# Kernel tuning notes

Measured on AMD Instinct MI355X. Metric: run time of the kernel, lower is better.

## Reference

```python
import jax, jax.numpy as jnp
import numpy as np

B, S, D, H = 4, 2048, 768, 12
DK = D // H


def setup_inputs() -> dict:
    key = jax.random.key(0)
    ks = jax.random.split(key, 5)
    sc = 0.02
    return {
        "x": jax.random.normal(ks[0], (B, S, D), dtype=jnp.float32),
        "wq": jax.random.normal(ks[1], (D, D), dtype=jnp.float32) * sc,
        "bq": jnp.zeros((D,), dtype=jnp.float32),
        "wk": jax.random.normal(ks[2], (D, D), dtype=jnp.float32) * sc,
        "bk": jnp.zeros((D,), dtype=jnp.float32),
        "wv": jax.random.normal(ks[3], (D, D), dtype=jnp.float32) * sc,
        "bv": jnp.zeros((D,), dtype=jnp.float32),
        "wo": jax.random.normal(ks[4], (D, D), dtype=jnp.float32) * sc,
        "bo": jnp.zeros((D,), dtype=jnp.float32),
    }


def reference(x, wq, bq, wk, bk, wv, bv, wo, bo):
    b, s, d = x.shape
    # torch nn.Linear: y = x @ W.T + b
    q = (x @ wq.T + bq).reshape(b, s, H, DK).transpose(0, 2, 1, 3)  # [b,h,s,dk]
    k = (x @ wk.T + bk).reshape(b, s, H, DK).transpose(0, 2, 1, 3)
    v = (x @ wv.T + bv).reshape(b, s, H, DK).transpose(0, 2, 1, 3)
    scale = 1.0 / np.sqrt(DK).astype(np.float32)
    scores = jnp.einsum("bhqd,bhkd->bhqk", q, k) * scale  # [b,h,s,s]
    causal = jnp.triu(jnp.ones((s, s), dtype=bool), k=1)  # True above diagonal -> masked
    scores = jnp.where(causal[None, None], jnp.float32(-jnp.inf), scores)
    probs = jax.nn.softmax(scores, axis=-1)
    attn = jnp.einsum("bhqk,bhkd->bhqd", probs, v)  # [b,h,s,dk]
    attn = attn.transpose(0, 2, 1, 3).reshape(b, s, d)
    return attn @ wo.T + bo
```

## Files before the change

kernel.cpp:

```cpp
#include <hip/hip_runtime.h>
#include <hip/hip_bf16.h>
#include <cstdint>

static constexpr int B_ = 4, S_ = 2048, D_ = 768, H_ = 12, DK_ = 64;
static constexpr int M_ = B_ * S_;

typedef short bf16x4 __attribute__((ext_vector_type(4)));
typedef short bf16x8 __attribute__((ext_vector_type(8)));
typedef float f32x4 __attribute__((ext_vector_type(4)));
typedef float f32x16 __attribute__((ext_vector_type(16)));
typedef int i32x4 __attribute__((ext_vector_type(4)));

#define MFMA16(a, b, c) __builtin_amdgcn_mfma_f32_16x16x32_bf16((a), (b), (c), 0, 0, 0)
#define MFMA32(a, b, c) __builtin_amdgcn_mfma_f32_32x32x16_bf16((a), (b), (c), 0, 0, 0)

__device__ inline ushort f2bf(float f) {
  uint32_t u = __float_as_uint(f);
  u += 0x7fffu + ((u >> 16) & 1u);
  return (ushort)(u >> 16);
}
__device__ inline uint32_t pkbf(float a, float b) {
  return (uint32_t)f2bf(a) | ((uint32_t)f2bf(b) << 16);
}
__device__ inline uint32_t cvtpk(float lo, float hi) {
  uint32_t r;
  asm("v_cvt_pk_bf16_f32 %0, %1, %2" : "=v"(r) : "v"(lo), "v"(hi));
  return r;
}
__device__ inline void gload_lds16(const void* g, void* l) {
  __builtin_amdgcn_global_load_lds((const __attribute__((address_space(1))) void*)g,
                                   (__attribute__((address_space(3))) void*)l, 16, 0, 0);
}

__global__ void cvt_f32_bf16(const float* __restrict__ in, ushort* __restrict__ out, int n8) {
  int i = blockIdx.x * 256 + threadIdx.x;
  if (i >= n8) return;
  const float4* p = (const float4*)in;
  float4 v0 = p[2 * i], v1 = p[2 * i + 1];
  ((uint4*)out)[i] = make_uint4(pkbf(v0.x, v0.y), pkbf(v0.z, v0.w),
                                pkbf(v1.x, v1.y), pkbf(v1.z, v1.w));
}

__global__ void cvtw_f32_bf16(const float* __restrict__ w0, const float* __restrict__ w1,
                              const float* __restrict__ w2, const float* __restrict__ w3,
                              ushort* __restrict__ o0, ushort* __restrict__ o1,
                              ushort* __restrict__ o2, ushort* __restrict__ o3, int n8) {
  const float* in;
  ushort* out;
  switch (blockIdx.y) {
    case 0: in = w0; out = o0; break;
    case 1: in = w1; out = o1; break;
    case 2: in = w2; out = o2; break;
    default: in = w3; out = o3; break;
  }
  int i = blockIdx.x * 256 + threadIdx.x;
  if (i >= n8) return;
  const float4* p = (const float4*)in;
  float4 v0 = p[2 * i], v1 = p[2 * i + 1];
  ((uint4*)out)[i] = make_uint4(pkbf(v0.x, v0.y), pkbf(v0.z, v0.w),
                                pkbf(v1.x, v1.y), pkbf(v1.z, v1.w));
}

__global__ __launch_bounds__(256) void gemm_qkv(const ushort* __restrict__ A,
                                                const ushort* __restrict__ Wq,
                                                const ushort* __restrict__ Wk,
                                                const ushort* __restrict__ Wv,
                                                const float* __restrict__ bqp,
                                                const float* __restrict__ bkp,
                                                const float* __restrict__ bvp,
                                                ushort* __restrict__ Qo,
                                                ushort* __restrict__ Ko,
                                                ushort* __restrict__ Vo) {
  constexpr int K = D_;
  constexpr int BK = 64;
  constexpr int NT = K / BK;
  __shared__ ushort SMEM[24576];
  ushort* Asb = SMEM;
  ushort* Bsb = SMEM + 8192;

  const int wsel = blockIdx.y / 6;
  const int bn = (blockIdx.y % 6) * 128;
  const ushort* Bw = wsel == 0 ? Wq : wsel == 1 ? Wk : Wv;
  const float* bias = wsel == 0 ? bqp : wsel == 1 ? bkp : bvp;
  ushort* outp = wsel == 0 ? Qo : wsel == 1 ? Ko : Vo;

  const int tid = threadIdx.x;
  const int lane = tid & 63, w = tid >> 6;
  const int wr = w >> 1, wc = w & 1;
  const int l15 = lane & 15, l4 = lane >> 4;
  const int bm = blockIdx.x * 64;

  const char* Ac = (const char*)A;
  const char* Bc = (const char*)Bw;

  f32x4 acc[2][4] = {};

  auto stage = [&](int buf, int k0) {
#pragma unroll
    for (int i = 0; i < 2; ++i) {
      int o = (i * 256 + tid) * 16;
      int r = o >> 7, c = o & 127;
      int cs = c ^ ((r & 7) << 4);
      gload_lds16(Ac + ((size_t)(bm + r) * K + k0) * 2 + cs,
                  (char*)(Asb + buf * 4096) + o);
    }
#pragma unroll
    for (int i = 0; i < 4; ++i) {
      int o = (i * 256 + tid) * 16;
      int r = o >> 7, c = o & 127;
      int cs = c ^ ((r & 7) << 4);
      gload_lds16(Bc + ((size_t)(bn + r) * K + k0) * 2 + cs,
                  (char*)(Bsb + buf * 8192) + o);
    }
  };

  stage(0, 0);
  __syncthreads();
  int cur = 0;
  for (int t = 0; t < NT; ++t) {
    if (t + 1 < NT) stage(cur ^ 1, (t + 1) * BK);
    const char* Ab = (const char*)(Asb + cur * 4096);
    const char* Bb = (const char*)(Bsb + cur * 8192);
    bf16x8 a[2][2], b[2][4];
#pragma unroll
    for (int kc = 0; kc < 2; ++kc) {
#pragma unroll
      for (int mi = 0; mi < 2; ++mi) {
        int row = wr * 32 + mi * 16 + l15;
        int col = (kc * 64 + l4 * 16) ^ ((row & 7) << 4);
        a[kc][mi] = *(const bf16x8*)(Ab + row * 128 + col);
      }
#pragma unroll
      for (int ni = 0; ni < 4; ++ni) {
        int row = wc * 64 + ni * 16 + l15;
        int col = (kc * 64 + l4 * 16) ^ ((row & 7) << 4);
        b[kc][ni] = *(const bf16x8*)(Bb + row * 128 + col);
      }
    }
    __builtin_amdgcn_s_setprio(1);
    if (wsel < 2) {
#pragma unroll
      for (int kc = 0; kc < 2; ++kc)
#pragma unroll
        for (int mi = 0; mi < 2; ++mi)
#pragma unroll
          for (int ni = 0; ni < 4; ++ni)
            acc[mi][ni] = MFMA16(a[kc][mi], b[kc][ni], acc[mi][ni]);
    } else {
#pragma unroll
      for (int kc = 0; kc < 2; ++kc)
#pragma unroll
        for (int mi = 0; mi < 2; ++mi)
#pragma unroll
          for (int ni = 0; ni < 4; ++ni)
            acc[mi][ni] = MFMA16(b[kc][ni], a[kc][mi], acc[mi][ni]);
    }
    __builtin_amdgcn_s_setprio(0);
    __syncthreads();
    cur ^= 1;
  }

  ushort* Cst = SMEM;
#pragma unroll
  for (int ni = 0; ni < 4; ++ni) {
    float bv[4];
    if (wsel < 2) {
      float bc = bias[bn + wc * 64 + ni * 16 + l15];
#pragma unroll
      for (int r = 0; r < 4; ++r) bv[r] = bc;
    } else {
#pragma unroll
      for (int r = 0; r < 4; ++r) bv[r] = bias[bn + wc * 64 + ni * 16 + l4 * 4 + r];
    }
#pragma unroll
    for (int mi = 0; mi < 2; ++mi)
#pragma unroll
      for (int r = 0; r < 4; ++r) {
        float v = acc[mi][ni][r] + bv[r];
        if (wsel < 2) {
          int lr = wr * 32 + mi * 16 + l4 * 4 + r;
          int lc = wc * 64 + ni * 16 + l15;
          Cst[lr * 128 + (lc ^ ((lr & 3) << 4))] = f2bf(v);
        } else {
          int lr = wc * 64 + ni * 16 + l4 * 4 + r;
          int lc = wr * 32 + mi * 16 + l15;
          Cst[lr * 64 + (lc ^ ((lr & 3) << 4))] = f2bf(v);
        }
      }
  }
  __syncthreads();
  const int bbV = bm >> 11;
#pragma unroll
  for (int it = 0; it < 4; ++it) {
    int chunk = it * 256 + tid;
    if (wsel < 2) {
      int lr = chunk >> 4, cc = chunk & 15;
      i32x4 v = *(const i32x4*)&Cst[lr * 128 + ((cc * 8) ^ ((lr & 3) << 4))];
      int gr = bm + lr;
      int b0 = gr >> 11, s = gr & 2047;
      int gc = bn + cc * 8;
      int h = gc >> 6, dk0 = gc & 63;
      *(i32x4*)&outp[((((size_t)b0 * H_ + h) * S_ + s) << 6) + dk0] = v;
    } else {
      int lr = chunk >> 3, cc = chunk & 7;
      i32x4 v = *(const i32x4*)&Cst[lr * 64 + ((cc * 8) ^ ((lr & 3) << 4))];
      int gn = bn + lr;
      int h = gn >> 6, dk = gn & 63;
      int s0 = (bm & 2047) + cc * 8;
      *(i32x4*)&outp[(((size_t)bbV * H_ + h) * 64 + dk) * S_ + s0] = v;
    }
  }
}

__global__ __launch_bounds__(256) void gemm_out(const ushort* __restrict__ A,
                                                const ushort* __restrict__ Bw,
                                                const float* __restrict__ bias,
                                                float* __restrict__ outp) {
  constexpr int K = D_;
  constexpr int BK = 32;
  constexpr int NT = K / BK;
  __shared__ ushort As[2][64 * BK];
  __shared__ ushort Bs[2][128 * BK];

  const int tid = threadIdx.x;
  const int lane = tid & 63, w = tid >> 6;
  const int wr = w >> 1, wc = w & 1;
  const int l15 = lane & 15, l4 = lane >> 4;
  const int bm = blockIdx.x * 64, bn = blockIdx.y * 128;

  f32x4 acc[2][4] = {};

  auto stage = [&](int buf, int k0) {
    {
      int e = tid * 8;
      int r = e >> 5, c = e & 31;
      gload_lds16(&A[(size_t)(bm + r) * K + k0 + c], &As[buf][e]);
    }
#pragma unroll
    for (int i = 0; i < 2; ++i) {
      int e = (i * 256 + tid) * 8;
      int r = e >> 5, c = e & 31;
      gload_lds16(&Bw[(size_t)(bn + r) * K + k0 + c], &Bs[buf][e]);
    }
  };

  stage(0, 0);
  __syncthreads();
  int cur = 0;
  for (int t = 0; t < NT; ++t) {
    if (t + 1 < NT) stage(cur ^ 1, (t + 1) * BK);
    bf16x8 a[2], b[4];
#pragma unroll
    for (int mi = 0; mi < 2; ++mi)
      a[mi] = *(const bf16x8*)&As[cur][(wr * 32 + mi * 16 + l15) * BK + l4 * 8];
#pragma unroll
    for (int ni = 0; ni < 4; ++ni)
      b[ni] = *(const bf16x8*)&Bs[cur][(wc * 64 + ni * 16 + l15) * BK + l4 * 8];
    __builtin_amdgcn_s_setprio(1);
#pragma unroll
    for (int mi = 0; mi < 2; ++mi)
#pragma unroll
      for (int ni = 0; ni < 4; ++ni)
        acc[mi][ni] = MFMA16(a[mi], b[ni], acc[mi][ni]);
    __builtin_amdgcn_s_setprio(0);
    __syncthreads();
    cur ^= 1;
  }

#pragma unroll
  for (int mi = 0; mi < 2; ++mi)
#pragma unroll
    for (int ni = 0; ni < 4; ++ni) {
      int col = bn + wc * 64 + ni * 16 + l15;
      float bv = bias[col];
#pragma unroll
      for (int r = 0; r < 4; ++r) {
        int row = bm + wr * 32 + mi * 16 + l4 * 4 + r;
        outp[(size_t)row * D_ + col] = acc[mi][ni][r] + bv;
      }
    }
}

__global__ __launch_bounds__(512) void attn_fwd5(const ushort* __restrict__ Q,
                                                 const ushort* __restrict__ Kg,
                                                 const ushort* __restrict__ Vt,
                                                 ushort* __restrict__ Oa) {
  __shared__ ushort KVb[2][2][64 * 64];
  __shared__ float Ml[4][32], Ll[4][32];

  const int bh = blockIdx.x;
  const int w = threadIdx.x >> 6, lane = threadIdx.x & 63;
  const int l31 = lane & 31, hi = lane >> 5;
  const int pair = w >> 1, sp = w & 1;
  const int qtb = gridDim.y - 1 - blockIdx.y;
  const int qb = qtb * 128;
  const int q0 = qb + pair * 32;

  const ushort* Qb = Q + (size_t)bh * (S_ * DK_);
  const char* Kc = (const char*)(Kg + (size_t)bh * (S_ * DK_));
  const char* Vc = (const char*)(Vt + (size_t)bh * (DK_ * S_));
  char* kKT = (char*)&KVb[0][0][0];
  char* kVT = (char*)&KVb[1][0][0];

  bf16x8 qf[4];
#pragma unroll
  for (int kc = 0; kc < 4; ++kc)
    qf[kc] = *(const bf16x8*)&Qb[(q0 + l31) * 64 + kc * 16 + hi * 8];

  f32x16 ot[2] = {};
  float m = -__builtin_inff(), l = 0.f;
  const float C = 0.125f * 1.4426950408889634f;
  const float THR = 8.0f / C;

  auto stage = [&](int buf, int kt) {
    const int k0 = kt * 64;
    int obase = w * 1024;
    int o = obase + lane * 16;
    int mk = ((o >> 7) & 7) << 4;
    gload_lds16(Kc + (size_t)k0 * 128 + (o ^ mk), kKT + buf * 8192 + obase);
    int d = o >> 7, colb = (o & 127) ^ mk;
    gload_lds16(Vc + (size_t)d * 4096 + (size_t)k0 * 2 + colb, kVT + buf * 8192 + obase);
  };

  const int nkt = qb / 64 + 2;
  int cur = 0;
  stage(0, 0);
  __syncthreads();

  for (int kt = 0; kt < nkt; ++kt) {
    if (kt + 1 < nkt) stage(cur ^ 1, kt + 1);
    const int ks = kt * 64 + sp * 32;
    if (ks <= q0 + 31) {
      const char* KTc = kKT + cur * 8192;
      const char* VTc = kVT + cur * 8192;
      f32x16 st = {};
      __builtin_amdgcn_s_setprio(1);
#pragma unroll
      for (int kc = 0; kc < 4; ++kc) {
        int row = sp * 32 + l31;
        int col = (kc * 32 + hi * 16) ^ ((row & 7) << 4);
        bf16x8 kf = *(const bf16x8*)(KTc + row * 128 + col);
        st = MFMA32(kf, qf[kc], st);
      }
      __builtin_amdgcn_s_setprio(0);
      if (ks + 31 > q0) {
#pragma unroll
        for (int r = 0; r < 16; ++r) {
          int kr = ks + (r & 3) + 8 * (r >> 2) + 4 * hi;
          if (kr > q0 + l31) st[r] = -__builtin_inff();
        }
      }
      float mx[8];
#pragma unroll
      for (int i = 0; i < 8; ++i) mx[i] = fmaxf(st[i], st[i + 8]);
#pragma unroll
      for (int i = 0; i < 4; ++i) mx[i] = fmaxf(mx[i], mx[i + 4]);
      float pm = fmaxf(fmaxf(mx[0], mx[1]), fmaxf(mx[2], mx[3]));
      pm = fmaxf(pm, __shfl_xor(pm, 32, 64));
      if (!__all(pm <= m + THR)) {
        float mn = fmaxf(m, pm);
        float al = exp2f((m - mn) * C);
        m = mn;
        l *= al;
#pragma unroll
        for (int t = 0; t < 2; ++t)
#pragma unroll
          for (int r = 0; r < 16; ++r) ot[t][r] *= al;
      }
      const float mc = m * C;
#pragma unroll
      for (int r = 0; r < 16; ++r) st[r] = exp2f(fmaf(st[r], C, -mc));
      float sx[8];
#pragma unroll
      for (int i = 0; i < 8; ++i) sx[i] = st[i] + st[i + 8];
#pragma unroll
      for (int i = 0; i < 4; ++i) sx[i] = sx[i] + sx[i + 4];
      float rs = (sx[0] + sx[1]) + (sx[2] + sx[3]);
      rs += __shfl_xor(rs, 32, 64);
      l += rs;
#pragma unroll
      for (int c = 0; c < 2; ++c) {
        i32x4 bw;
        bw.x = (int)cvtpk(st[8 * c + 0], st[8 * c + 1]);
        bw.y = (int)cvtpk(st[8 * c + 2], st[8 * c + 3]);
        bw.z = (int)cvtpk(st[8 * c + 4], st[8 * c + 5]);
        bw.w = (int)cvtpk(st[8 * c + 6], st[8 * c + 7]);
        bf16x8 pf = __builtin_bit_cast(bf16x8, bw);
        __builtin_amdgcn_s_setprio(1);
#pragma unroll
        for (int t = 0; t < 2; ++t) {
          int row = t * 32 + l31;
          int swz = (row & 7) << 4;
          int colA = sp * 64 + c * 32 + hi * 8;
          bf16x4 vlo = *(const bf16x4*)(VTc + row * 128 + (colA ^ swz));
          bf16x4 vhi = *(const bf16x4*)(VTc + row * 128 + ((colA + 16) ^ swz));
          bf16x8 vf = __builtin_shufflevector(vlo, vhi, 0, 1, 2, 3, 4, 5, 6, 7);
          ot[t] = MFMA32(vf, pf, ot[t]);
        }
        __builtin_amdgcn_s_setprio(0);
      }
    }
    __syncthreads();
    cur ^= 1;
  }

  float* Om = (float*)&KVb[0][0][0];
  if (sp == 0) {
#pragma unroll
    for (int t = 0; t < 2; ++t)
#pragma unroll
      for (int r = 0; r < 16; ++r) {
        int d = (r & 3) + 8 * (r >> 2) + 4 * hi + 32 * t;
        Om[(pair * 64 + d) * 32 + l31] = ot[t][r];
      }
    if (hi == 0) { Ml[pair][l31] = m; Ll[pair][l31] = l; }
  }
  __syncthreads();
  if (sp == 1) {
    float m0 = Ml[pair][l31], l0 = Ll[pair][l31];
    float M = fmaxf(m, m0);
    float a1 = exp2f((m - M) * C), a0 = exp2f((m0 - M) * C);
    float inv = 1.0f / (a1 * l + a0 * l0);
    a1 *= inv; a0 *= inv;
#pragma unroll
    for (int t = 0; t < 2; ++t)
#pragma unroll
      for (int r = 0; r < 16; ++r) {
        int d = (r & 3) + 8 * (r >> 2) + 4 * hi + 32 * t;
        ot[t][r] = a1 * ot[t][r] + a0 * Om[(pair * 64 + d) * 32 + l31];
      }
    uint32_t* Ow = (uint32_t*)&Om[pair * 64 * 32];
#pragma unroll
    for (int t = 0; t < 2; ++t)
#pragma unroll
      for (int g = 0; g < 4; ++g)
#pragma unroll
        for (int rp = 0; rp < 2; ++rp) {
          int r0 = 4 * g + 2 * rp;
          int ucol = rp + 4 * g + 2 * hi + 16 * t;
          Ow[l31 * 32 + (ucol ^ ((l31 & 7) << 2))] = cvtpk(ot[t][r0], ot[t][r0 + 1]);
        }
    const int bb = bh / H_, h = bh % H_;
#pragma unroll
    for (int i = 0; i < 4; ++i) {
      int chunk = i * 64 + lane;
      int q = chunk >> 3, cc = chunk & 7;
      i32x4 v = *(const i32x4*)&Ow[q * 32 + ((cc * 4) ^ ((q & 7) << 2))];
      *(i32x4*)&Oa[((size_t)bb * S_ + q0 + q) * D_ + h * 64 + cc * 8] = v;
    }
  }
}

extern "C" void kernel_launch(void* const* d_in, const int* in_sizes, int n_in,
                              void* d_out, int out_size, void* d_ws, size_t ws_size,
                              hipStream_t stream) {
  const float* x  = (const float*)d_in[0];
  const float* wq = (const float*)d_in[1];
  const float* bq = (const float*)d_in[2];
  const float* wk = (const float*)d_in[3];
  const float* bk = (const float*)d_in[4];
  const float* wv = (const float*)d_in[5];
  const float* bv = (const float*)d_in[6];
  const float* wo = (const float*)d_in[7];
  const float* bo = (const float*)d_in[8];

  const size_t XB = (size_t)M_ * D_;
  const size_t WB = (size_t)D_ * D_;
  ushort* xb    = (ushort*)d_ws;
  ushort* wqb   = xb + XB;
  ushort* wkb   = wqb + WB;
  ushort* wvb   = wkb + WB;
  ushort* wob   = wvb + WB;
  ushort* qb    = wob + WB;
  ushort* kbuf  = qb + XB;
  ushort* vtb   = kbuf + XB;
  ushort* attnb = vtb + XB;

  cvt_f32_bf16<<<(int)(XB / 8 / 256), 256, 0, stream>>>(x, xb, (int)(XB / 8));
  cvtw_f32_bf16<<<dim3((int)(WB / 8 / 256), 4), 256, 0, stream>>>(
      wq, wk, wv, wo, wqb, wkb, wvb, wob, (int)(WB / 8));

  gemm_qkv<<<dim3(M_ / 64, 18), 256, 0, stream>>>(xb, wqb, wkb, wvb,
                                                  bq, bk, bv, qb, kbuf, vtb);
  attn_fwd5<<<dim3(B_ * H_, S_ / 128), 512, 0, stream>>>(qb, kbuf, vtb, attnb);
  gemm_out<<<dim3(M_ / 64, D_ / 128), 256, 0, stream>>>(attnb, wob, bo, (float*)d_out);
}
```

Baseline: 127.6 us.

## Double gemm_out K-tile with swizzled LDS and halve attention query tile

gemm_out now stages K tiles of 64 instead of 32. Its LDS reads and writes use an XOR swizzle to avoid bank conflicts, and it issues twice as many MFMAs per barrier. The attention kernel moves from 128-query blocks of 8 waves to 64-query blocks of 4 waves, launching twice as many blocks for better load balance across CUs on the causal workload. Each thread now stages two K/V chunks per tile. Smaller attention blocks reload K/V tiles more often, raising memory traffic.

```diff
diff --git a/kernel.cpp b/kernel.cpp
--- a/kernel.cpp
+++ b/kernel.cpp
@@ -217,10 +217,11 @@
                                                 const float* __restrict__ bias,
                                                 float* __restrict__ outp) {
   constexpr int K = D_;
-  constexpr int BK = 32;
+  constexpr int BK = 64;
   constexpr int NT = K / BK;
-  __shared__ ushort As[2][64 * BK];
-  __shared__ ushort Bs[2][128 * BK];
+  __shared__ ushort SMEM[24576];
+  ushort* Asb = SMEM;
+  ushort* Bsb = SMEM + 8192;
 
   const int tid = threadIdx.x;
   const int lane = tid & 63, w = tid >> 6;
@@ -228,19 +229,27 @@
   const int l15 = lane & 15, l4 = lane >> 4;
   const int bm = blockIdx.x * 64, bn = blockIdx.y * 128;
 
+  const char* Ac = (const char*)A;
+  const char* Bc = (const char*)Bw;
+
   f32x4 acc[2][4] = {};
 
   auto stage = [&](int buf, int k0) {
-    {
-      int e = tid * 8;
-      int r = e >> 5, c = e & 31;
-      gload_lds16(&A[(size_t)(bm + r) * K + k0 + c], &As[buf][e]);
-    }
 #pragma unroll
     for (int i = 0; i < 2; ++i) {
-      int e = (i * 256 + tid) * 8;
-      int r = e >> 5, c = e & 31;
-      gload_lds16(&Bw[(size_t)(bn + r) * K + k0 + c], &Bs[buf][e]);
+      int o = (i * 256 + tid) * 16;
+      int r = o >> 7, c = o & 127;
+      int cs = c ^ ((r & 7) << 4);
+      gload_lds16(Ac + ((size_t)(bm + r) * K + k0) * 2 + cs,
+                  (char*)(Asb + buf * 4096) + o);
+    }
+#pragma unroll
+    for (int i = 0; i < 4; ++i) {
+      int o = (i * 256 + tid) * 16;
+      int r = o >> 7, c = o & 127;
+      int cs = c ^ ((r & 7) << 4);
+      gload_lds16(Bc + ((size_t)(bn + r) * K + k0) * 2 + cs,
+                  (char*)(Bsb + buf * 8192) + o);
     }
   };
 
@@ -249,19 +258,32 @@
   int cur = 0;
   for (int t = 0; t < NT; ++t) {
     if (t + 1 < NT) stage(cur ^ 1, (t + 1) * BK);
-    bf16x8 a[2], b[4];
-#pragma unroll
-    for (int mi = 0; mi < 2; ++mi)
-      a[mi] = *(const bf16x8*)&As[cur][(wr * 32 + mi * 16 + l15) * BK + l4 * 8];
-#pragma unroll
-    for (int ni = 0; ni < 4; ++ni)
-      b[ni] = *(const bf16x8*)&Bs[cur][(wc * 64 + ni * 16 + l15) * BK + l4 * 8];
+    const char* Ab = (const char*)(Asb + cur * 4096);
+    const char* Bb = (const char*)(Bsb + cur * 8192);
+    bf16x8 a[2][2], b[2][4];
+#pragma unroll
+    for (int kc = 0; kc < 2; ++kc) {
+#pragma unroll
+      for (int mi = 0; mi < 2; ++mi) {
+        int row = wr * 32 + mi * 16 + l15;
+        int col = (kc * 64 + l4 * 16) ^ ((row & 7) << 4);
+        a[kc][mi] = *(const bf16x8*)(Ab + row * 128 + col);
+      }
+#pragma unroll
+      for (int ni = 0; ni < 4; ++ni) {
+        int row = wc * 64 + ni * 16 + l15;
+        int col = (kc * 64 + l4 * 16) ^ ((row & 7) << 4);
+        b[kc][ni] = *(const bf16x8*)(Bb + row * 128 + col);
+      }
+    }
     __builtin_amdgcn_s_setprio(1);
 #pragma unroll
-    for (int mi = 0; mi < 2; ++mi)
-#pragma unroll
-      for (int ni = 0; ni < 4; ++ni)
-        acc[mi][ni] = MFMA16(a[mi], b[ni], acc[mi][ni]);
+    for (int kc = 0; kc < 2; ++kc)
+#pragma unroll
+      for (int mi = 0; mi < 2; ++mi)
+#pragma unroll
+        for (int ni = 0; ni < 4; ++ni)
+          acc[mi][ni] = MFMA16(a[kc][mi], b[kc][ni], acc[mi][ni]);
     __builtin_amdgcn_s_setprio(0);
     __syncthreads();
     cur ^= 1;
@@ -281,19 +303,19 @@
     }
 }
 
-__global__ __launch_bounds__(512) void attn_fwd5(const ushort* __restrict__ Q,
+__global__ __launch_bounds__(256) void attn_fwd6(const ushort* __restrict__ Q,
                                                  const ushort* __restrict__ Kg,
                                                  const ushort* __restrict__ Vt,
                                                  ushort* __restrict__ Oa) {
   __shared__ ushort KVb[2][2][64 * 64];
-  __shared__ float Ml[4][32], Ll[4][32];
+  __shared__ float Ml[2][32], Ll[2][32];
 
   const int bh = blockIdx.x;
   const int w = threadIdx.x >> 6, lane = threadIdx.x & 63;
   const int l31 = lane & 31, hi = lane >> 5;
   const int pair = w >> 1, sp = w & 1;
   const int qtb = gridDim.y - 1 - blockIdx.y;
-  const int qb = qtb * 128;
+  const int qb = qtb * 64;
   const int q0 = qb + pair * 32;
 
   const ushort* Qb = Q + (size_t)bh * (S_ * DK_);
@@ -314,15 +336,19 @@
 
   auto stage = [&](int buf, int kt) {
     const int k0 = kt * 64;
-    int obase = w * 1024;
-    int o = obase + lane * 16;
-    int mk = ((o >> 7) & 7) << 4;
-    gload_lds16(Kc + (size_t)k0 * 128 + (o ^ mk), kKT + buf * 8192 + obase);
-    int d = o >> 7, colb = (o & 127) ^ mk;
-    gload_lds16(Vc + (size_t)d * 4096 + (size_t)k0 * 2 + colb, kVT + buf * 8192 + obase);
+#pragma unroll
+    for (int i = 0; i < 2; ++i) {
+      int obase = w * 2048 + i * 1024;
+      int o = obase + lane * 16;
+      int mk = ((o >> 7) & 7) << 4;
+      gload_lds16(Kc + (size_t)k0 * 128 + (o ^ mk), kKT + buf * 8192 + obase);
+      int d = o >> 7, colb = (o & 127) ^ mk;
+      gload_lds16(Vc + (size_t)d * 4096 + (size_t)k0 * 2 + colb,
+                  kVT + buf * 8192 + obase);
+    }
   };
 
-  const int nkt = qb / 64 + 2;
+  const int nkt = qb / 64 + 1;
   int cur = 0;
   stage(0, 0);
   __syncthreads();
@@ -482,6 +508,6 @@
 
   gemm_qkv<<<dim3(M_ / 64, 18), 256, 0, stream>>>(xb, wqb, wkb, wvb,
                                                   bq, bk, bv, qb, kbuf, vtb);
-  attn_fwd5<<<dim3(B_ * H_, S_ / 128), 512, 0, stream>>>(qb, kbuf, vtb, attnb);
+  attn_fwd6<<<dim3(B_ * H_, S_ / 64), 256, 0, stream>>>(qb, kbuf, vtb, attnb);
   gemm_out<<<dim3(M_ / 64, D_ / 128), 256, 0, stream>>>(attnb, wob, bo, (float*)d_out);
 }
```

After: 135.1 us. 1.06x slower.
